# Kernel tuning notes

Hardware: AMD Instinct MI355X
Metric: run time of the kernel (lower is better)

## Reference

```python
import jax, jax.numpy as jnp
import numpy as np

B, S, HID = 2, 2048, 2048
H, D = 16, 128
BASE = 10000.0
NEG = -1e9


def _rope_tables(seq_len, dim, dtype):
    inv_freq = 1.0 / (BASE ** (jnp.arange(0, dim, 2, dtype=jnp.float32) / dim))
    pos = jnp.arange(seq_len, dtype=jnp.float32)
    freqs = jnp.einsum('s,d->sd', pos, inv_freq)          # [S, D/2]
    emb = jnp.concatenate([freqs, freqs], axis=-1)        # [S, D]
    return jnp.cos(emb).astype(dtype), jnp.sin(emb).astype(dtype)


def _rotate_half(x):
    x1, x2 = jnp.split(x, 2, axis=-1)
    return jnp.concatenate([-x2, x1], axis=-1)


def setup_inputs() -> dict:
    key = jax.random.key(0)
    k1, k2, k3 = jax.random.split(key, 3)
    x = jax.random.normal(k1, (B, S, HID), dtype=jnp.float32)
    w_qkv = jax.random.normal(k2, (HID, 3 * HID), dtype=jnp.float32) * (HID ** -0.5)
    w_out = jax.random.normal(k3, (HID, HID), dtype=jnp.float32) * (HID ** -0.5)
    return {"x": x, "w_qkv": w_qkv, "w_out": w_out}


def reference(x, w_qkv, w_out):
    b, s, _ = x.shape
    qkv = x @ w_qkv                                        # [B, S, 3*HID]
    qkv = qkv.reshape(b, s, 3, H, D).transpose(2, 0, 3, 1, 4)  # [3, B, H, S, D]
    q, k, v = qkv[0], qkv[1], qkv[2]
    cos, sin = _rope_tables(s, D, x.dtype)                 # [S, D]
    cos = cos[None, None]
    sin = sin[None, None]
    q = q * cos + _rotate_half(q) * sin
    k = k * cos + _rotate_half(k) * sin
    scale = 1.0 / np.sqrt(D)
    scores = jnp.einsum('bhqd,bhkd->bhqk', q, k) * scale   # [B, H, S, S]
    causal = jnp.triu(jnp.ones((s, s), dtype=bool), k=1)
    scores = jnp.where(causal[None, None], NEG, scores)
    attn = jax.nn.softmax(scores, axis=-1)
    out = jnp.einsum('bhqk,bhkd->bhqd', attn, v)           # [B, H, S, D]
    out = out.transpose(0, 2, 1, 3).reshape(b, s, H * D)
    return out @ w_out
```

## Files before the change

### kernel.cpp

```cpp
#include <hip/hip_runtime.h>
#include <hip/hip_bf16.h>

#define S_LEN 2048
#define HID_DIM 2048
#define NH 16
#define HD 128
#define N3 6144

typedef __bf16 bf16x8 __attribute__((ext_vector_type(8)));
typedef unsigned short u16x8 __attribute__((ext_vector_type(8)));
typedef float f32x4 __attribute__((ext_vector_type(4)));
typedef float f32x16 __attribute__((ext_vector_type(16)));

#define MFMA16(a, b, c) __builtin_amdgcn_mfma_f32_16x16x32_bf16(a, b, c, 0, 0, 0)
#define MFMA32(a, b, c) __builtin_amdgcn_mfma_f32_32x32x16_bf16(a, b, c, 0, 0, 0)

__device__ __forceinline__ unsigned short f2bf(float f) {
  union { float f; unsigned u; } v; v.f = f;
  return (unsigned short)((v.u + 0x7fffu + ((v.u >> 16) & 1u)) >> 16);
}
__device__ __forceinline__ float bf2f(unsigned short h) {
  union { unsigned u; float f; } v; v.u = ((unsigned)h) << 16; return v.f;
}
__device__ __forceinline__ unsigned packbf2(float lo, float hi) {
  union { __hip_bfloat162 h2; unsigned u; } cv;
  cv.h2 = __float22bfloat162_rn(make_float2(lo, hi));
  return cv.u;
}
__device__ __forceinline__ void store_c(float* p, float v) { *p = v; }
__device__ __forceinline__ void store_c(unsigned short* p, float v) { *p = f2bf(v); }

__device__ __forceinline__ float fexp2(float x) {
  float r; asm("v_exp_f32 %0, %1" : "=v"(r) : "v"(x)); return r;
}

__device__ __forceinline__ void async16(const void* g, void* l) {
  __builtin_amdgcn_global_load_lds((const __attribute__((address_space(1))) unsigned int*)g,
                                   (__attribute__((address_space(3))) unsigned int*)l,
                                   16, 0, 0);
}

template <int N> __device__ __forceinline__ void vmcnt();
template <> __device__ __forceinline__ void vmcnt<0>() { asm volatile("s_waitcnt vmcnt(0)" ::: "memory"); }
template <> __device__ __forceinline__ void vmcnt<5>() { asm volatile("s_waitcnt vmcnt(5)" ::: "memory"); }
template <> __device__ __forceinline__ void vmcnt<6>() { asm volatile("s_waitcnt vmcnt(6)" ::: "memory"); }

#define PLSWAP(a, b) asm volatile("v_permlane32_swap_b32 %0, %1" : "+v"(a), "+v"(b))

__global__ __launch_bounds__(256) void prep_all(const float4* __restrict__ x4,
                                                ushort4* __restrict__ xb4,
                                                const float* __restrict__ w_qkv,
                                                unsigned short* __restrict__ wqkvT,
                                                const float* __restrict__ w_out,
                                                unsigned short* __restrict__ woutT,
                                                float* __restrict__ cosT,
                                                float* __restrict__ sinT) {
  __shared__ float t[32][33];
  int bid = blockIdx.x;
  const int tid = threadIdx.x;

  if (bid < 8192) {
    int i = bid * 256 + tid;
    float4 v = x4[i];
    ushort4 o;
    o.x = f2bf(v.x); o.y = f2bf(v.y); o.z = f2bf(v.z); o.w = f2bf(v.w);
    xb4[i] = o;
    return;
  }
  bid -= 8192;
  if (bid < 12288 + 4096) {
    const float* src; unsigned short* dst; int R, Ccols;
    if (bid < 12288) { src = w_qkv; dst = wqkvT; R = 2048; Ccols = 6144; }
    else { bid -= 12288; src = w_out; dst = woutT; R = 2048; Ccols = 2048; }
    int ct = Ccols >> 5;
    int bx = bid % ct, by = bid / ct;
    int c0 = bx << 5, r0 = by << 5;
    int lx = tid & 31, ly = tid >> 5;
#pragma unroll
    for (int i = 0; i < 32; i += 8)
      t[ly + i][lx] = src[(long long)(r0 + ly + i) * Ccols + c0 + lx];
    __syncthreads();
    {
      const int j = tid >> 3;
      const int seg = tid & 7;
      ushort4 o;
      o.x = f2bf(t[seg * 4 + 0][j]);
      o.y = f2bf(t[seg * 4 + 1][j]);
      o.z = f2bf(t[seg * 4 + 2][j]);
      o.w = f2bf(t[seg * 4 + 3][j]);
      *(ushort4*)(dst + (long long)(c0 + j) * R + r0 + seg * 4) = o;
    }
    return;
  }
  bid -= 16384;
  int idx = bid * 256 + tid;
  int s = idx >> 6, i = idx & 63;
  float invf = powf(10000.0f, -(float)i * (1.0f / 64.0f));
  float a = (float)s * invf;
  cosT[idx] = cosf(a);
  sinT[idx] = sinf(a);
}

__global__ __launch_bounds__(512) void gemm256_rope(const unsigned short* __restrict__ A,
                                                    const unsigned short* __restrict__ Bt,
                                                    unsigned short* __restrict__ Qb,
                                                    unsigned short* __restrict__ Kb,
                                                    const float* __restrict__ cosT,
                                                    const float* __restrict__ sinT,
                                                    int Mdim, int Ncols, int Kdim) {
  constexpr int AEL = 256 * 64, BUFE = 2 * AEL;
  __shared__ unsigned short smem[2 * BUFE];

  const int ntn = Ncols >> 8;
  const int nwg = (Mdim >> 8) * ntn;
  int bid = blockIdx.x;
  bid = (bid & 7) * (nwg >> 3) + (bid >> 3);
  const int tm = (bid / ntn) << 8;
  const int tn = (bid % ntn) << 8;

  const int tid = threadIdx.x;
  const int w = tid >> 6, l = tid & 63;
  const int g = l >> 4, cc = l & 15;
  const int wm = w >> 2, wn = w & 3;

  const int srow = tid >> 3;
  const int schunk = (tid & 7) ^ (srow & 7);
  const unsigned short* gA = A + (long long)(tm + srow) * Kdim + schunk * 8;
  const unsigned short* gB = Bt + (long long)(tn + srow) * Kdim + schunk * 8;

  const int ch0 = ((g) ^ (cc & 7)) << 3;
  const int ch1 = ((4 + g) ^ (cc & 7)) << 3;

  f32x4 acc[8][4] = {};
  bf16x8 a[4][2], b[4][2];
  const int nk = Kdim >> 6;

#define ST_A(kt2, BUF, s) \
  async16(gA + (long long)(s) * 64 * Kdim + ((long long)(kt2) << 6), \
          smem + (BUF) * BUFE + (s) * 4096 + w * 512)
#define ST_B(kt2, BUF, s) \
  async16(gB + (long long)(s) * 64 * Kdim + ((long long)(kt2) << 6), \
          smem + (BUF) * BUFE + AEL + (s) * 4096 + w * 512)

#pragma unroll
  for (int s = 0; s < 4; ++s) ST_A(0, 0, s);
#pragma unroll
  for (int s = 0; s < 4; ++s) ST_B(0, 0, s);
  ST_A(1, 1, 0); ST_A(1, 1, 2);
  ST_B(1, 1, 0); ST_B(1, 1, 1); ST_B(1, 1, 2); ST_B(1, 1, 3);
  vmcnt<6>();
  __builtin_amdgcn_s_barrier();

#define KSTEP(kt, BUF, OBUF)                                                      \
  {                                                                               \
    const unsigned short* Ab = smem + (BUF) * BUFE + wm * (128 * 64);             \
    const unsigned short* Bb = smem + (BUF) * BUFE + AEL + wn * (64 * 64);        \
                    \
    _Pragma("unroll") for (int i = 0; i < 4; ++i) {                               \
      const int r = (i * 16 + cc) << 6;                                           \
      a[i][0] = *(const bf16x8*)(Ab + r + ch0);                                   \
      a[i][1] = *(const bf16x8*)(Ab + r + ch1);                                   \
    }                                                                             \
    _Pragma("unroll") for (int j = 0; j < 2; ++j) {                               \
      const int r = (j * 16 + cc) << 6;                                           \
      b[j][0] = *(const bf16x8*)(Bb + r + ch0);                                   \
      b[j][1] = *(const bf16x8*)(Bb + r + ch1);                                   \
    }                                                                             \
    if ((kt) + 1 < nk) { ST_A((kt) + 1, OBUF, 1); ST_A((kt) + 1, OBUF, 3); }      \
    __builtin_amdgcn_s_barrier();                                                 \
    __builtin_amdgcn_s_setprio(1);                                                \
    _Pragma("unroll") for (int i = 0; i < 4; ++i)                                 \
      _Pragma("unroll") for (int j = 0; j < 2; ++j) {                             \
        acc[i][j] = MFMA16(a[i][0], b[j][0], acc[i][j]);                          \
        acc[i][j] = MFMA16(a[i][1], b[j][1], acc[i][j]);                          \
      }                                                                           \
    __builtin_amdgcn_s_setprio(0);                                                \
    __builtin_amdgcn_s_barrier();                                                 \
                                              \
    _Pragma("unroll") for (int j = 0; j < 2; ++j) {                               \
      const int r = ((2 + j) * 16 + cc) << 6;                                     \
      b[2 + j][0] = *(const bf16x8*)(Bb + r + ch0);                               \
      b[2 + j][1] = *(const bf16x8*)(Bb + r + ch1);                               \
    }                                                                             \
    if ((kt) + 2 < nk) { ST_A((kt) + 2, BUF, 0); ST_A((kt) + 2, BUF, 2); }        \
    __builtin_amdgcn_s_barrier();                                                 \
    __builtin_amdgcn_s_setprio(1);                                                \
    _Pragma("unroll") for (int i = 0; i < 4; ++i)                                 \
      _Pragma("unroll") for (int j = 0; j < 2; ++j) {                             \
        acc[i][2 + j] = MFMA16(a[i][0], b[2 + j][0], acc[i][2 + j]);              \
        acc[i][2 + j] = MFMA16(a[i][1], b[2 + j][1], acc[i][2 + j]);              \
      }                                                                           \
    __builtin_amdgcn_s_setprio(0);                                                \
    __builtin_amdgcn_s_barrier();                                                 \
                                              \
    _Pragma("unroll") for (int i = 0; i < 4; ++i) {                               \
      const int r = ((64 + i * 16 + cc) << 6);                                    \
      a[i][0] = *(const bf16x8*)(Ab + r + ch0);                                   \
      a[i][1] = *(const bf16x8*)(Ab + r + ch1);                                   \
    }                                                                             \
    if ((kt) + 2 < nk) { ST_B((kt) + 2, BUF, 0); ST_B((kt) + 2, BUF, 1); }        \
    __builtin_amdgcn_s_barrier();                                                 \
    __builtin_amdgcn_s_setprio(1);                                                \
    _Pragma("unroll") for (int i = 0; i < 4; ++i)                                 \
      _Pragma("unroll") for (int j = 0; j < 2; ++j) {                             \
        acc[4 + i][j] = MFMA16(a[i][0], b[j][0], acc[4 + i][j]);                  \
        acc[4 + i][j] = MFMA16(a[i][1], b[j][1], acc[4 + i][j]);                  \
      }                                                                           \
    __builtin_amdgcn_s_setprio(0);                                                \
    __builtin_amdgcn_s_barrier();                                                 \
                            \
    if ((kt) + 2 < nk) { ST_B((kt) + 2, BUF, 2); ST_B((kt) + 2, BUF, 3); }        \
    __builtin_amdgcn_s_barrier();                                                 \
    __builtin_amdgcn_s_setprio(1);                                                \
    _Pragma("unroll") for (int i = 0; i < 4; ++i)                                 \
      _Pragma("unroll") for (int j = 0; j < 2; ++j) {                             \
        acc[4 + i][2 + j] = MFMA16(a[i][0], b[2 + j][0], acc[4 + i][2 + j]);      \
        acc[4 + i][2 + j] = MFMA16(a[i][1], b[2 + j][1], acc[4 + i][2 + j]);      \
      }                                                                           \
    __builtin_amdgcn_s_setprio(0);                                                \
    if ((kt) + 2 < nk) vmcnt<6>(); else vmcnt<0>();                               \
    __builtin_amdgcn_s_barrier();                                                 \
  }

  for (int kt = 0; kt < nk; kt += 2) {
    KSTEP(kt, 0, 1);
    KSTEP(kt + 1, 1, 0);
  }
#undef KSTEP
#undef ST_A
#undef ST_B

  const bool isQ = tn < 2048;
  unsigned short* qkout = isQ ? Qb : Kb;
  const float scl = isQ ? (0.08838834764831845f * 1.4426950408889634f) : 1.0f;
  const int colbase = tn & 2047;
  __syncthreads();
#pragma unroll
  for (int pass = 0; pass < 2; ++pass) {
    if (wm == pass) {
#pragma unroll
      for (int i = 0; i < 8; ++i)
#pragma unroll
        for (int j = 0; j < 4; ++j)
#pragma unroll
          for (int p = 0; p < 4; ++p)
            smem[(i * 16 + (g << 2) + p) * 264 + wn * 64 + j * 16 + cc] = f2bf(acc[i][j][p]);
    }
    __syncthreads();
    {
      const int r = tid >> 2;
      const int c0 = (tid & 3) << 6;
      const int grow = tm + (pass << 7) + r;
      const int bb = grow >> 11, ss = grow & 2047;
      const float* cpb = cosT + (ss << 6);
      const float* spb = sinT + (ss << 6);
#pragma unroll
      for (int k2 = 0; k2 < 8; ++k2) {
        const int c = c0 + (k2 << 3);
        const int gcol = colbase + c;
        const int hh = gcol >> 7, dd = gcol & 127;
        u16x8 v = *(const u16x8*)(smem + r * 264 + c);
        u16x8 pr = *(const u16x8*)(smem + r * 264 + (c ^ 64));
        const int d6 = dd & 63;
        f32x4 ca = *(const f32x4*)(cpb + d6), cb = *(const f32x4*)(cpb + d6 + 4);
        f32x4 sa4 = *(const f32x4*)(spb + d6), sb4 = *(const f32x4*)(spb + d6 + 4);
        const float sgn = (dd < 64) ? -1.0f : 1.0f;
        u16x8 o;
#pragma unroll
        for (int e = 0; e < 8; ++e) {
          float cv = (e < 4) ? ca[e & 3] : cb[e & 3];
          float sv = (e < 4) ? sa4[e & 3] : sb4[e & 3];
          o[e] = f2bf((bf2f(v[e]) * cv + sgn * bf2f(pr[e]) * sv) * scl);
        }
        *(u16x8*)(qkout + ((long long)((bb * NH + hh) * S_LEN + ss) * HD + dd)) = o;
      }
    }
    __syncthreads();
  }
}

template <int BM, int BN, typename OutT, bool VTOUT = false>
__global__ __launch_bounds__(512) void gemm_pipe8(const unsigned short* __restrict__ A,
                                                  const unsigned short* __restrict__ Bt,
                                                  OutT* __restrict__ C,
                                                  int Mdim, int Ncols, int ldc, int Kdim) {
  constexpr int WTM = BM / 2, WTN = BN / 4;
  constexpr int MREP = WTM / 16, NREP = WTN / 16;
  constexpr int AEL = BM * 64, BEL = BN * 64, BUFE = AEL + BEL;
  constexpr int AINST = BM / 64, BINST = BN / 64;
  constexpr int AHALF = BM / 128, BHALF = BN / 128;
  constexpr int VN = BN / 64 + BM / 128;
  __shared__ unsigned short smem[2 * BUFE];

  const int ntn = Ncols / BN;
  const int nwg = (Mdim / BM) * ntn;
  int bid = blockIdx.x;
  bid = (bid & 7) * (nwg >> 3) + (bid >> 3);
  const int tm = (bid / ntn) * BM;
  const int tn = (bid % ntn) * BN;

  const int tid = threadIdx.x;
  const int w = tid >> 6, l = tid & 63;
  const int g = l >> 4, cc = l & 15;
  const int wm = w >> 2, wn = w & 3;

  const int srow = tid >> 3;
  const int schunk = (tid & 7) ^ (srow & 7);
  const unsigned short* gA = A + (long long)(tm + srow) * Kdim + schunk * 8;
  const unsigned short* gB = Bt + (long long)(tn + srow) * Kdim + schunk * 8;

  const int ch0 = ((g) ^ (cc & 7)) << 3;
  const int ch1 = ((4 + g) ^ (cc & 7)) << 3;

  f32x4 acc[MREP][NREP] = {};
  bf16x8 a[MREP / 2][2], b[NREP][2];

  const int nk = Kdim >> 6;

#define STAGE_A(kt2, s) \
  async16(gA + (long long)(s) * 64 * Kdim + ((long long)(kt2) << 6), \
          smem + ((kt2) & 1) * BUFE + (s) * 4096 + w * 512)
#define STAGE_B(kt2, s) \
  async16(gB + (long long)(s) * 64 * Kdim + ((long long)(kt2) << 6), \
          smem + ((kt2) & 1) * BUFE + AEL + (s) * 4096 + w * 512)

#pragma unroll
  for (int s = 0; s < AINST; ++s) STAGE_A(0, s);
#pragma unroll
  for (int s = 0; s < BINST; ++s) STAGE_B(0, s);
#pragma unroll
  for (int s = 0; s < BINST; ++s) STAGE_B(1, s);
#pragma unroll
  for (int s = 0; s < AHALF; ++s) STAGE_A(1, s);
  vmcnt<VN>();
  __builtin_amdgcn_s_barrier();

  for (int kt = 0; kt < nk; ++kt) {
    const int buf = kt & 1;
    const unsigned short* Ab = smem + buf * BUFE + (wm * WTM) * 64;
    const unsigned short* Bb = smem + buf * BUFE + AEL + (wn * WTN) * 64;

#pragma unroll
    for (int i = 0; i < MREP / 2; ++i) {
      const int r = (i * 16 + cc) << 6;
      a[i][0] = *(const bf16x8*)(Ab + r + ch0);
      a[i][1] = *(const bf16x8*)(Ab + r + ch1);
    }
#pragma unroll
    for (int j = 0; j < NREP; ++j) {
      const int r = (j * 16 + cc) << 6;
      b[j][0] = *(const bf16x8*)(Bb + r + ch0);
      b[j][1] = *(const bf16x8*)(Bb + r + ch1);
    }
    if (kt + 1 < nk) {
#pragma unroll
      for (int s = AHALF; s < AINST; ++s) STAGE_A(kt + 1, s);
    }
    __builtin_amdgcn_s_barrier();
    __builtin_amdgcn_s_setprio(1);
#pragma unroll
    for (int i = 0; i < MREP / 2; ++i)
#pragma unroll
      for (int j = 0; j < NREP / 2; ++j) {
        acc[i][j] = MFMA16(a[i][0], b[j][0], acc[i][j]);
        acc[i][j] = MFMA16(a[i][1], b[j][1], acc[i][j]);
      }
    __builtin_amdgcn_s_setprio(0);
    __builtin_amdgcn_s_barrier();

    if (kt + 2 < nk) {
#pragma unroll
      for (int s = 0; s < BHALF; ++s) STAGE_B(kt + 2, s);
    }
    __builtin_amdgcn_s_barrier();
    __builtin_amdgcn_s_setprio(1);
#pragma unroll
    for (int i = 0; i < MREP / 2; ++i)
#pragma unroll
      for (int j = 0; j < NREP / 2; ++j) {
        f32x4& ac = acc[i][NREP / 2 + j];
        ac = MFMA16(a[i][0], b[NREP / 2 + j][0], ac);
        ac = MFMA16(a[i][1], b[NREP / 2 + j][1], ac);
      }
    __builtin_amdgcn_s_setprio(0);
    __builtin_amdgcn_s_barrier();

#pragma unroll
    for (int i = 0; i < MREP / 2; ++i) {
      const int r = ((WTM / 2) + i * 16 + cc) << 6;
      a[i][0] = *(const bf16x8*)(Ab + r + ch0);
      a[i][1] = *(const bf16x8*)(Ab + r + ch1);
    }
    if (kt + 2 < nk) {
#pragma unroll
      for (int s = BHALF; s < BINST; ++s) STAGE_B(kt + 2, s);
    }
    __builtin_amdgcn_s_barrier();
    __builtin_amdgcn_s_setprio(1);
#pragma unroll
    for (int i = 0; i < MREP / 2; ++i)
#pragma unroll
      for (int j = 0; j < NREP / 2; ++j) {
        f32x4& ac = acc[MREP / 2 + i][j];
        ac = MFMA16(a[i][0], b[j][0], ac);
        ac = MFMA16(a[i][1], b[j][1], ac);
      }
    __builtin_amdgcn_s_setprio(0);
    __builtin_amdgcn_s_barrier();

    if (kt + 2 < nk) {
#pragma unroll
      for (int s = 0; s < AHALF; ++s) STAGE_A(kt + 2, s);
    }
    __builtin_amdgcn_s_barrier();
    __builtin_amdgcn_s_setprio(1);
#pragma unroll
    for (int i = 0; i < MREP / 2; ++i)
#pragma unroll
      for (int j = 0; j < NREP / 2; ++j) {
        f32x4& ac = acc[MREP / 2 + i][NREP / 2 + j];
        ac = MFMA16(a[i][0], b[NREP / 2 + j][0], ac);
        ac = MFMA16(a[i][1], b[NREP / 2 + j][1], ac);
      }
    __builtin_amdgcn_s_setprio(0);
    if (kt + 2 < nk) vmcnt<VN>(); else vmcnt<0>();
    __builtin_amdgcn_s_barrier();
  }
#undef STAGE_A
#undef STAGE_B

  const int crow0 = tm + wm * WTM;
  const int ccol0 = tn + wn * WTN;
  if constexpr (VTOUT) {
    unsigned short* Vt = (unsigned short*)C;
#pragma unroll
    for (int i = 0; i < MREP; ++i)
#pragma unroll
      for (int j = 0; j < NREP; ++j) {
        int col = ccol0 + j * 16 + cc;
        int rowb = crow0 + i * 16 + (g << 2);
        long long vt = ((long long)(((rowb >> 11) << 4) + (col >> 7)) * 128 + (col & 127)) * 2048 +
                       (rowb & 2047);
        ushort4 o;
        o.x = f2bf(acc[i][j][0]); o.y = f2bf(acc[i][j][1]);
        o.z = f2bf(acc[i][j][2]); o.w = f2bf(acc[i][j][3]);
        *(ushort4*)(Vt + vt) = o;
      }
  } else {
#pragma unroll
    for (int i = 0; i < MREP; ++i)
#pragma unroll
      for (int j = 0; j < NREP; ++j)
#pragma unroll
        for (int p = 0; p < 4; ++p) {
          int row = crow0 + i * 16 + (g << 2) + p;
          int col = ccol0 + j * 16 + cc;
          store_c(&C[(long long)row * ldc + col], acc[i][j][p]);
        }
  }
}

__global__ __launch_bounds__(256) void flash_attn(const unsigned short* __restrict__ Qg,
                                                  const unsigned short* __restrict__ Kg,
                                                  const unsigned short* __restrict__ Vt,
                                                  unsigned short* __restrict__ Ob) {
  __shared__ unsigned short smem[32768];
  const int id = blockIdx.x;
  const int bh = id & 31;
  const int qtr = (id >> 5) & 7;
  const int qt = (id >> 8) ? qtr : 15 - qtr;
  const int Q0 = qt << 7;
  const int b = bh >> 4, h = bh & 15;
  const long long base = (long long)bh * (S_LEN * HD);
  const int tid = threadIdx.x, w = tid >> 6, l = tid & 63;
  const int hi = l >> 5, q = l & 31;
  const int q0w = Q0 + (w << 5);
  const int g = l >> 4, c = l & 15;

  bf16x8 qf[8];
  {
    const unsigned short* qp = Qg + base + (long long)(q0w + q) * HD + (hi << 3);
#pragma unroll
    for (int s = 0; s < 8; ++s) qf[s] = *(const bf16x8*)(qp + (s << 4));
  }

  f32x16 oacc[4] = {};
  float m = -1e30f, lsum = 0.f;

  const int nt = (qt << 1) + 2;

  auto STAGE = [&](int kv0, int buf) {
    unsigned short* ks = smem + buf * 8192;
    unsigned short* vs = smem + 16384 + buf * 8192;
#pragma unroll
    for (int j = 0; j < 4; ++j) {
      int row = (w << 4) + (j << 2) + g;
      int chunk = c ^ (row & 15);
      async16(Kg + base + (long long)(kv0 + row) * HD + (chunk << 3),
              ks + (((w << 4) + (j << 2)) << 7));
    }
#pragma unroll
    for (int j = 0; j < 4; ++j) {
      int dr = (w << 5) + (j << 3) + (l >> 3);
      int chunk = (l & 7) ^ (dr & 7);
      async16(Vt + base + (long long)dr * S_LEN + kv0 + (chunk << 3),
              vs + (((w << 5) + (j << 3)) << 6));
    }
  };

  STAGE(0, 0);
  __syncthreads();

  int cur = 0;
  for (int t = 0; t < nt; ++t) {
    const int kv0 = t << 6;
    if (t + 1 < nt) STAGE((t + 1) << 6, cur ^ 1);

    if (kv0 < q0w + 32) {
      const unsigned short* ks = smem + cur * 8192;
      const unsigned short* vs = smem + 16384 + cur * 8192;

      f32x16 sa[2] = {};
#pragma unroll
      for (int h2 = 0; h2 < 2; ++h2) {
        const char* kb = (const char*)ks + (((h2 << 5) + q) << 8);
        const int rm = q & 15;
#pragma unroll
        for (int s = 0; s < 8; ++s) {
          bf16x8 kf = *(const bf16x8*)(kb + ((((s << 1) + hi) ^ rm) << 4));
          sa[h2] = MFMA32(kf, qf[s], sa[h2]);
        }
      }

      if (kv0 + 63 > q0w) {
        const int qq = q0w + q;
#pragma unroll
        for (int h2 = 0; h2 < 2; ++h2)
#pragma unroll
          for (int j = 0; j < 16; ++j) {
            int kv = kv0 + (h2 << 5) + (j & 3) + ((j >> 2) << 3) + (hi << 2);
            if (kv > qq) sa[h2][j] = -1e30f;
          }
      }

      float t0 = sa[0][0], t1 = sa[0][1], t2 = sa[0][2], t3 = sa[0][3];
#pragma unroll
      for (int j = 4; j < 16; j += 4) {
        t0 = fmaxf(t0, sa[0][j]);     t1 = fmaxf(t1, sa[0][j + 1]);
        t2 = fmaxf(t2, sa[0][j + 2]); t3 = fmaxf(t3, sa[0][j + 3]);
      }
#pragma unroll
      for (int j = 0; j < 16; j += 4) {
        t0 = fmaxf(t0, sa[1][j]);     t1 = fmaxf(t1, sa[1][j + 1]);
        t2 = fmaxf(t2, sa[1][j + 2]); t3 = fmaxf(t3, sa[1][j + 3]);
      }
      float tmax = fmaxf(fmaxf(t0, t1), fmaxf(t2, t3));
      {
        float tcp;
        asm volatile("v_mov_b32 %0, %1" : "=v"(tcp) : "v"(tmax));
        PLSWAP(tmax, tcp);
        tmax = fmaxf(tmax, tcp);
      }
      float mn = fmaxf(m, tmax);
      float fsc = fexp2(m - mn);
      m = mn;
      float s0 = 0.f, s1 = 0.f, s2 = 0.f, s3 = 0.f;
#pragma unroll
      for (int h2 = 0; h2 < 2; ++h2)
#pragma unroll
        for (int j = 0; j < 16; j += 4) {
          float p0 = fexp2(sa[h2][j] - mn);
          float p1 = fexp2(sa[h2][j + 1] - mn);
          float p2 = fexp2(sa[h2][j + 2] - mn);
          float p3 = fexp2(sa[h2][j + 3] - mn);
          sa[h2][j] = p0; sa[h2][j + 1] = p1;
          sa[h2][j + 2] = p2; sa[h2][j + 3] = p3;
          s0 += p0; s1 += p1; s2 += p2; s3 += p3;
        }
      float ps = (s0 + s1) + (s2 + s3);
      {
        float pcp;
        asm volatile("v_mov_b32 %0, %1" : "=v"(pcp) : "v"(ps));
        PLSWAP(ps, pcp);
        ps = ps + pcp;
      }
      lsum = lsum * fsc + ps;
#pragma unroll
      for (int db = 0; db < 4; ++db)
#pragma unroll
        for (int j = 0; j < 16; ++j) oacc[db][j] *= fsc;

      unsigned up[2][8];
#pragma unroll
      for (int h2 = 0; h2 < 2; ++h2)
#pragma unroll
        for (int k = 0; k < 8; ++k)
          up[h2][k] = packbf2(sa[h2][2 * k], sa[h2][2 * k + 1]);
      union Frag { unsigned u[4]; bf16x8 v; } pf[4];
#pragma unroll
      for (int s = 0; s < 4; ++s) {
        int h2 = s >> 1, q4 = (s & 1) << 2;
        unsigned a0 = up[h2][q4 + 0], b0 = up[h2][q4 + 2];
        unsigned a1 = up[h2][q4 + 1], b1 = up[h2][q4 + 3];
        PLSWAP(a0, b0);
        PLSWAP(a1, b1);
        pf[s].u[0] = a0; pf[s].u[1] = a1;
        pf[s].u[2] = b0; pf[s].u[3] = b1;
      }

#pragma unroll
      for (int db = 0; db < 4; ++db) {
        const char* vb = (const char*)vs + (((db << 5) + q) << 7);
        const int d7 = q & 7;
#pragma unroll
        for (int s = 0; s < 4; ++s) {
          bf16x8 vf = *(const bf16x8*)(vb + ((((s << 1) + hi) ^ d7) << 4));
          oacc[db] = MFMA32(vf, pf[s].v, oacc[db]);
        }
      }
    }

    __syncthreads();
    cur ^= 1;
  }

  const float rl = 1.0f / lsum;
#pragma unroll
  for (int db = 0; db < 4; ++db)
#pragma unroll
    for (int jg = 0; jg < 4; ++jg) {
      int d = (db << 5) + (jg << 3) + (hi << 2);
      unsigned v0 = packbf2(oacc[db][4 * jg] * rl, oacc[db][4 * jg + 1] * rl);
      unsigned v1 = packbf2(oacc[db][4 * jg + 2] * rl, oacc[db][4 * jg + 3] * rl);
      *(uint2*)(smem + (((w << 5) + q) << 7) + d) = make_uint2(v0, v1);
    }
  __syncthreads();
  {
    const int qr = tid >> 1;
    const int dh = (tid & 1) << 6;
    const uint4* src = (const uint4*)(smem + (qr << 7) + dh);
    uint4* dst = (uint4*)(Ob + (long long)((b << 11) + Q0 + qr) * HID_DIM + (h << 7) + dh);
#pragma unroll
    for (int cc2 = 0; cc2 < 8; ++cc2) dst[cc2] = src[cc2];
  }
}

extern "C" void kernel_launch(void* const* d_in, const int* in_sizes, int n_in,
                              void* d_out, int out_size, void* d_ws, size_t ws_size,
                              hipStream_t stream) {
  (void)in_sizes; (void)n_in; (void)out_size; (void)ws_size;
  const float* x = (const float*)d_in[0];
  const float* w_qkv = (const float*)d_in[1];
  const float* w_out = (const float*)d_in[2];
  float* out = (float*)d_out;
  char* ws = (char*)d_ws;

  unsigned short* xb    = (unsigned short*)(ws);
  unsigned short* wqkvT = (unsigned short*)(ws + 16777216);
  unsigned short* woutT = (unsigned short*)(ws + 41943040);
  unsigned short* qkv   = (unsigned short*)(ws + 50331648);
  unsigned short* Qb    = (unsigned short*)(ws + 100663296);
  unsigned short* Kb    = (unsigned short*)(ws + 117440512);
  unsigned short* Vt    = (unsigned short*)(ws + 134217728);
  float* cosT = (float*)(ws + 150994944);
  float* sinT = (float*)(ws + 151519232);
  unsigned short* Ob = qkv;

  prep_all<<<25088, 256, 0, stream>>>((const float4*)x, (ushort4*)xb,
                                      w_qkv, wqkvT, w_out, woutT, cosT, sinT);
  gemm256_rope<<<256, 512, 0, stream>>>(xb, wqkvT, Qb, Kb, cosT, sinT, 4096, 4096, 2048);
  gemm_pipe8<128, 256, unsigned short, true><<<256, 512, 0, stream>>>(
      xb, wqkvT + (long long)4096 * 2048, Vt, 4096, 2048, 2048, 2048);
  flash_attn<<<512, 256, 0, stream>>>(Qb, Kb, Vt, Ob);
  gemm_pipe8<128, 256, float><<<256, 512, 0, stream>>>(Ob, woutT, out, 4096, 2048, 2048, 2048);
}
```

Before: 254.8 us.

## Retile QK GEMM warps per head so RoPE epilogue runs from registers

Changes the QKV projection GEMM warp layout from a 2x4 to a 4x2 grid, so each warp owns 64 rows by 128 columns, which is one full head. The rotate-half partner of each column (d and d+64) then sits in the same thread's accumulators. The RoPE epilogue is computed straight from those registers. This removes the LDS staging pass, its bf16 round trip and several __syncthreads. The async load order is reshuffled so shared buffers are overwritten only after the new read pattern has finished with them. In exchange, output writes become scalar 2-byte stores instead of 16-byte vector stores, the cos/sin lookups are scalar, and the MFMA fragment mix shifts toward more B fragments held per warp.

```diff
diff --git a/kernel.cpp b/kernel.cpp
--- a/kernel.cpp
+++ b/kernel.cpp
@@ -121,7 +121,7 @@
   const int tid = threadIdx.x;
   const int w = tid >> 6, l = tid & 63;
   const int g = l >> 4, cc = l & 15;
-  const int wm = w >> 2, wn = w & 3;
+  const int wm = w >> 1, wn = w & 1;
 
   const int srow = tid >> 3;
   const int schunk = (tid & 7) ^ (srow & 7);
@@ -131,8 +131,8 @@
   const int ch0 = ((g) ^ (cc & 7)) << 3;
   const int ch1 = ((4 + g) ^ (cc & 7)) << 3;
 
-  f32x4 acc[8][4] = {};
-  bf16x8 a[4][2], b[4][2];
+  f32x4 acc[4][8] = {};
+  bf16x8 a[2][2], b[8][2];
   const int nk = Kdim >> 6;
 
 #define ST_A(kt2, BUF, s) \
@@ -153,15 +153,15 @@
 
 #define KSTEP(kt, BUF, OBUF)                                                      \
   {                                                                               \
-    const unsigned short* Ab = smem + (BUF) * BUFE + wm * (128 * 64);             \
-    const unsigned short* Bb = smem + (BUF) * BUFE + AEL + wn * (64 * 64);        \
-                    \
-    _Pragma("unroll") for (int i = 0; i < 4; ++i) {                               \
+    const unsigned short* Ab = smem + (BUF) * BUFE + wm * (64 * 64);              \
+    const unsigned short* Bb = smem + (BUF) * BUFE + AEL + wn * (128 * 64);       \
+             \
+    _Pragma("unroll") for (int i = 0; i < 2; ++i) {                               \
       const int r = (i * 16 + cc) << 6;                                           \
       a[i][0] = *(const bf16x8*)(Ab + r + ch0);                                   \
       a[i][1] = *(const bf16x8*)(Ab + r + ch1);                                   \
     }                                                                             \
-    _Pragma("unroll") for (int j = 0; j < 2; ++j) {                               \
+    _Pragma("unroll") for (int j = 0; j < 4; ++j) {                               \
       const int r = (j * 16 + cc) << 6;                                           \
       b[j][0] = *(const bf16x8*)(Bb + r + ch0);                                   \
       b[j][1] = *(const bf16x8*)(Bb + r + ch1);                                   \
@@ -169,53 +169,53 @@
     if ((kt) + 1 < nk) { ST_A((kt) + 1, OBUF, 1); ST_A((kt) + 1, OBUF, 3); }      \
     __builtin_amdgcn_s_barrier();                                                 \
     __builtin_amdgcn_s_setprio(1);                                                \
-    _Pragma("unroll") for (int i = 0; i < 4; ++i)                                 \
-      _Pragma("unroll") for (int j = 0; j < 2; ++j) {                             \
+    _Pragma("unroll") for (int i = 0; i < 2; ++i)                                 \
+      _Pragma("unroll") for (int j = 0; j < 4; ++j) {                             \
         acc[i][j] = MFMA16(a[i][0], b[j][0], acc[i][j]);                          \
         acc[i][j] = MFMA16(a[i][1], b[j][1], acc[i][j]);                          \
       }                                                                           \
     __builtin_amdgcn_s_setprio(0);                                                \
     __builtin_amdgcn_s_barrier();                                                 \
-                                              \
-    _Pragma("unroll") for (int j = 0; j < 2; ++j) {                               \
-      const int r = ((2 + j) * 16 + cc) << 6;                                     \
-      b[2 + j][0] = *(const bf16x8*)(Bb + r + ch0);                               \
-      b[2 + j][1] = *(const bf16x8*)(Bb + r + ch1);                               \
+                    \
+    _Pragma("unroll") for (int j = 0; j < 4; ++j) {                               \
+      const int r = (((4 + j) * 16 + cc) << 6);                                   \
+      b[4 + j][0] = *(const bf16x8*)(Bb + r + ch0);                               \
+      b[4 + j][1] = *(const bf16x8*)(Bb + r + ch1);                               \
     }                                                                             \
-    if ((kt) + 2 < nk) { ST_A((kt) + 2, BUF, 0); ST_A((kt) + 2, BUF, 2); }        \
+    if ((kt) + 2 < nk) { ST_B((kt) + 2, BUF, 0); ST_B((kt) + 2, BUF, 2); }        \
     __builtin_amdgcn_s_barrier();                                                 \
     __builtin_amdgcn_s_setprio(1);                                                \
-    _Pragma("unroll") for (int i = 0; i < 4; ++i)                                 \
-      _Pragma("unroll") for (int j = 0; j < 2; ++j) {                             \
-        acc[i][2 + j] = MFMA16(a[i][0], b[2 + j][0], acc[i][2 + j]);              \
-        acc[i][2 + j] = MFMA16(a[i][1], b[2 + j][1], acc[i][2 + j]);              \
+    _Pragma("unroll") for (int i = 0; i < 2; ++i)                                 \
+      _Pragma("unroll") for (int j = 0; j < 4; ++j) {                             \
+        acc[i][4 + j] = MFMA16(a[i][0], b[4 + j][0], acc[i][4 + j]);              \
+        acc[i][4 + j] = MFMA16(a[i][1], b[4 + j][1], acc[i][4 + j]);              \
       }                                                                           \
     __builtin_amdgcn_s_setprio(0);                                                \
     __builtin_amdgcn_s_barrier();                                                 \
-                                              \
-    _Pragma("unroll") for (int i = 0; i < 4; ++i) {                               \
-      const int r = ((64 + i * 16 + cc) << 6);                                    \
+                    \
+    _Pragma("unroll") for (int i = 0; i < 2; ++i) {                               \
+      const int r = ((32 + i * 16 + cc) << 6);                                    \
       a[i][0] = *(const bf16x8*)(Ab + r + ch0);                                   \
       a[i][1] = *(const bf16x8*)(Ab + r + ch1);                                   \
     }                                                                             \
-    if ((kt) + 2 < nk) { ST_B((kt) + 2, BUF, 0); ST_B((kt) + 2, BUF, 1); }        \
+    if ((kt) + 2 < nk) { ST_B((kt) + 2, BUF, 1); ST_B((kt) + 2, BUF, 3); }        \
     __builtin_amdgcn_s_barrier();                                                 \
     __builtin_amdgcn_s_setprio(1);                                                \
-    _Pragma("unroll") for (int i = 0; i < 4; ++i)                                 \
-      _Pragma("unroll") for (int j = 0; j < 2; ++j) {                             \
-        acc[4 + i][j] = MFMA16(a[i][0], b[j][0], acc[4 + i][j]);                  \
-        acc[4 + i][j] = MFMA16(a[i][1], b[j][1], acc[4 + i][j]);                  \
+    _Pragma("unroll") for (int i = 0; i < 2; ++i)                                 \
+      _Pragma("unroll") for (int j = 0; j < 4; ++j) {                             \
+        acc[2 + i][j] = MFMA16(a[i][0], b[j][0], acc[2 + i][j]);                  \
+        acc[2 + i][j] = MFMA16(a[i][1], b[j][1], acc[2 + i][j]);                  \
       }                                                                           \
     __builtin_amdgcn_s_setprio(0);                                                \
     __builtin_amdgcn_s_barrier();                                                 \
-                            \
-    if ((kt) + 2 < nk) { ST_B((kt) + 2, BUF, 2); ST_B((kt) + 2, BUF, 3); }        \
+                 \
+    if ((kt) + 2 < nk) { ST_A((kt) + 2, BUF, 0); ST_A((kt) + 2, BUF, 2); }        \
     __builtin_amdgcn_s_barrier();                                                 \
     __builtin_amdgcn_s_setprio(1);                                                \
-    _Pragma("unroll") for (int i = 0; i < 4; ++i)                                 \
-      _Pragma("unroll") for (int j = 0; j < 2; ++j) {                             \
-        acc[4 + i][2 + j] = MFMA16(a[i][0], b[2 + j][0], acc[4 + i][2 + j]);      \
-        acc[4 + i][2 + j] = MFMA16(a[i][1], b[2 + j][1], acc[4 + i][2 + j]);      \
+    _Pragma("unroll") for (int i = 0; i < 2; ++i)                                 \
+      _Pragma("unroll") for (int j = 0; j < 4; ++j) {                             \
+        acc[2 + i][4 + j] = MFMA16(a[i][0], b[4 + j][0], acc[2 + i][4 + j]);      \
+        acc[2 + i][4 + j] = MFMA16(a[i][1], b[4 + j][1], acc[2 + i][4 + j]);      \
       }                                                                           \
     __builtin_amdgcn_s_setprio(0);                                                \
     if ((kt) + 2 < nk) vmcnt<6>(); else vmcnt<0>();                               \
@@ -233,50 +233,26 @@
   const bool isQ = tn < 2048;
   unsigned short* qkout = isQ ? Qb : Kb;
   const float scl = isQ ? (0.08838834764831845f * 1.4426950408889634f) : 1.0f;
-  const int colbase = tn & 2047;
-  __syncthreads();
-#pragma unroll
-  for (int pass = 0; pass < 2; ++pass) {
-    if (wm == pass) {
-#pragma unroll
-      for (int i = 0; i < 8; ++i)
-#pragma unroll
-        for (int j = 0; j < 4; ++j)
-#pragma unroll
-          for (int p = 0; p < 4; ++p)
-            smem[(i * 16 + (g << 2) + p) * 264 + wn * 64 + j * 16 + cc] = f2bf(acc[i][j][p]);
-    }
-    __syncthreads();
-    {
-      const int r = tid >> 2;
-      const int c0 = (tid & 3) << 6;
-      const int grow = tm + (pass << 7) + r;
-      const int bb = grow >> 11, ss = grow & 2047;
+  const int hh = ((tn & 2047) >> 7) + wn;
+  const int rowb0 = tm + wm * 64;
+#pragma unroll
+  for (int i = 0; i < 4; ++i)
+#pragma unroll
+    for (int p = 0; p < 4; ++p) {
+      const int row = rowb0 + i * 16 + (g << 2) + p;
+      const int bb = row >> 11, ss = row & 2047;
+      const long long obase = ((long long)((bb * NH + hh) * S_LEN + ss)) * HD;
       const float* cpb = cosT + (ss << 6);
       const float* spb = sinT + (ss << 6);
 #pragma unroll
-      for (int k2 = 0; k2 < 8; ++k2) {
-        const int c = c0 + (k2 << 3);
-        const int gcol = colbase + c;
-        const int hh = gcol >> 7, dd = gcol & 127;
-        u16x8 v = *(const u16x8*)(smem + r * 264 + c);
-        u16x8 pr = *(const u16x8*)(smem + r * 264 + (c ^ 64));
-        const int d6 = dd & 63;
-        f32x4 ca = *(const f32x4*)(cpb + d6), cb = *(const f32x4*)(cpb + d6 + 4);
-        f32x4 sa4 = *(const f32x4*)(spb + d6), sb4 = *(const f32x4*)(spb + d6 + 4);
-        const float sgn = (dd < 64) ? -1.0f : 1.0f;
-        u16x8 o;
-#pragma unroll
-        for (int e = 0; e < 8; ++e) {
-          float cv = (e < 4) ? ca[e & 3] : cb[e & 3];
-          float sv = (e < 4) ? sa4[e & 3] : sb4[e & 3];
-          o[e] = f2bf((bf2f(v[e]) * cv + sgn * bf2f(pr[e]) * sv) * scl);
-        }
-        *(u16x8*)(qkout + ((long long)((bb * NH + hh) * S_LEN + ss) * HD + dd)) = o;
-      }
-    }
-    __syncthreads();
-  }
+      for (int j = 0; j < 4; ++j) {
+        const int dlo = j * 16 + cc;
+        const float cv = cpb[dlo], sv = spb[dlo];
+        const float lo = acc[i][j][p], hi = acc[i][j + 4][p];
+        qkout[obase + dlo] = f2bf((lo * cv - hi * sv) * scl);
+        qkout[obase + dlo + 64] = f2bf((hi * cv + lo * sv) * scl);
+      }
+    }
 }
 
 template <int BM, int BN, typename OutT, bool VTOUT = false>
```

Result: faster. 247.7 us (-2.8%).

## Remap B-tile columns per wave so RoPE pairs stay in registers

Applied to the files above, without the earlier changes.

Changes which B rows each wave reads so that a wave's accumulator holds both halves (d and d+64) of its head's dimensions. RoPE can then be applied straight from registers, with no bf16 staging through shared memory and none of the extra barriers. The cost is that global stores become scattered 2-byte writes instead of 16-byte vector writes. The math also changes slightly, since rotation now runs on fp32 accumulators before any bf16 rounding.

```diff
diff --git a/kernel.cpp b/kernel.cpp
--- a/kernel.cpp
+++ b/kernel.cpp
@@ -131,6 +131,7 @@
   const int ch0 = ((g) ^ (cc & 7)) << 3;
   const int ch1 = ((4 + g) ^ (cc & 7)) << 3;
 
+  const int bbase = ((wn >> 1) << 7) + ((wn & 1) << 5);
   f32x4 acc[8][4] = {};
   bf16x8 a[4][2], b[4][2];
   const int nk = Kdim >> 6;
@@ -154,15 +155,15 @@
 #define KSTEP(kt, BUF, OBUF)                                                      \
   {                                                                               \
     const unsigned short* Ab = smem + (BUF) * BUFE + wm * (128 * 64);             \
-    const unsigned short* Bb = smem + (BUF) * BUFE + AEL + wn * (64 * 64);        \
-                    \
+    const unsigned short* Bb = smem + (BUF) * BUFE + AEL;                         \
+                \
     _Pragma("unroll") for (int i = 0; i < 4; ++i) {                               \
       const int r = (i * 16 + cc) << 6;                                           \
       a[i][0] = *(const bf16x8*)(Ab + r + ch0);                                   \
       a[i][1] = *(const bf16x8*)(Ab + r + ch1);                                   \
     }                                                                             \
     _Pragma("unroll") for (int j = 0; j < 2; ++j) {                               \
-      const int r = (j * 16 + cc) << 6;                                           \
+      const int r = ((bbase + j * 16 + cc) << 6);                                 \
       b[j][0] = *(const bf16x8*)(Bb + r + ch0);                                   \
       b[j][1] = *(const bf16x8*)(Bb + r + ch1);                                   \
     }                                                                             \
@@ -176,9 +177,9 @@
       }                                                                           \
     __builtin_amdgcn_s_setprio(0);                                                \
     __builtin_amdgcn_s_barrier();                                                 \
-                                              \
+                                          \
     _Pragma("unroll") for (int j = 0; j < 2; ++j) {                               \
-      const int r = ((2 + j) * 16 + cc) << 6;                                     \
+      const int r = ((bbase + 64 + j * 16 + cc) << 6);                            \
       b[2 + j][0] = *(const bf16x8*)(Bb + r + ch0);                               \
       b[2 + j][1] = *(const bf16x8*)(Bb + r + ch1);                               \
     }                                                                             \
@@ -192,7 +193,7 @@
       }                                                                           \
     __builtin_amdgcn_s_setprio(0);                                                \
     __builtin_amdgcn_s_barrier();                                                 \
-                                              \
+                                          \
     _Pragma("unroll") for (int i = 0; i < 4; ++i) {                               \
       const int r = ((64 + i * 16 + cc) << 6);                                    \
       a[i][0] = *(const bf16x8*)(Ab + r + ch0);                                   \
@@ -208,7 +209,7 @@
       }                                                                           \
     __builtin_amdgcn_s_setprio(0);                                                \
     __builtin_amdgcn_s_barrier();                                                 \
-                            \
+                        \
     if ((kt) + 2 < nk) { ST_B((kt) + 2, BUF, 2); ST_B((kt) + 2, BUF, 3); }        \
     __builtin_amdgcn_s_barrier();                                                 \
     __builtin_amdgcn_s_setprio(1);                                                \
@@ -233,50 +234,27 @@
   const bool isQ = tn < 2048;
   unsigned short* qkout = isQ ? Qb : Kb;
   const float scl = isQ ? (0.08838834764831845f * 1.4426950408889634f) : 1.0f;
-  const int colbase = tn & 2047;
-  __syncthreads();
-#pragma unroll
-  for (int pass = 0; pass < 2; ++pass) {
-    if (wm == pass) {
-#pragma unroll
-      for (int i = 0; i < 8; ++i)
-#pragma unroll
-        for (int j = 0; j < 4; ++j)
-#pragma unroll
-          for (int p = 0; p < 4; ++p)
-            smem[(i * 16 + (g << 2) + p) * 264 + wn * 64 + j * 16 + cc] = f2bf(acc[i][j][p]);
-    }
-    __syncthreads();
-    {
-      const int r = tid >> 2;
-      const int c0 = (tid & 3) << 6;
-      const int grow = tm + (pass << 7) + r;
-      const int bb = grow >> 11, ss = grow & 2047;
+  const int hh = ((tn & 2047) >> 7) + (wn >> 1);
+  const int dbase = ((wn & 1) << 5);
+  const int crow0 = tm + wm * 128;
+#pragma unroll
+  for (int i = 0; i < 8; ++i)
+#pragma unroll
+    for (int p = 0; p < 4; ++p) {
+      const int row = crow0 + i * 16 + (g << 2) + p;
+      const int bb = row >> 11, ss = row & 2047;
+      const long long obase = ((long long)((bb * NH + hh) * S_LEN + ss)) * HD;
       const float* cpb = cosT + (ss << 6);
       const float* spb = sinT + (ss << 6);
 #pragma unroll
-      for (int k2 = 0; k2 < 8; ++k2) {
-        const int c = c0 + (k2 << 3);
-        const int gcol = colbase + c;
-        const int hh = gcol >> 7, dd = gcol & 127;
-        u16x8 v = *(const u16x8*)(smem + r * 264 + c);
-        u16x8 pr = *(const u16x8*)(smem + r * 264 + (c ^ 64));
-        const int d6 = dd & 63;
-        f32x4 ca = *(const f32x4*)(cpb + d6), cb = *(const f32x4*)(cpb + d6 + 4);
-        f32x4 sa4 = *(const f32x4*)(spb + d6), sb4 = *(const f32x4*)(spb + d6 + 4);
-        const float sgn = (dd < 64) ? -1.0f : 1.0f;
-        u16x8 o;
-#pragma unroll
-        for (int e = 0; e < 8; ++e) {
-          float cv = (e < 4) ? ca[e & 3] : cb[e & 3];
-          float sv = (e < 4) ? sa4[e & 3] : sb4[e & 3];
-          o[e] = f2bf((bf2f(v[e]) * cv + sgn * bf2f(pr[e]) * sv) * scl);
-        }
-        *(u16x8*)(qkout + ((long long)((bb * NH + hh) * S_LEN + ss) * HD + dd)) = o;
-      }
-    }
-    __syncthreads();
-  }
+      for (int j = 0; j < 2; ++j) {
+        const int dlo = dbase + j * 16 + cc;
+        const float cv = cpb[dlo], sv = spb[dlo];
+        const float lo = acc[i][j][p], hi = acc[i][j + 2][p];
+        qkout[obase + dlo] = f2bf((lo * cv - hi * sv) * scl);
+        qkout[obase + dlo + 64] = f2bf((hi * cv + lo * sv) * scl);
+      }
+    }
 }
 
 template <int BM, int BN, typename OutT, bool VTOUT = false>
```

After: 245.8 us. 1.04x faster.
